# Performance work log

Hardware: AMD Instinct MI355X
Metric: run time of the kernel (lower is better)

The kernel has to match this reference:

```python
import jax, jax.numpy as jnp
import numpy as np
from jax.ops import segment_sum

N = 100000   # nodes
E = 6400000  # edges
D = 128      # input/output feature dim (d)
H = 15       # hidden width hard-coded in the module


def setup_inputs() -> dict:
    key = jax.random.key(0)
    ks = jax.random.split(key, 10)
    x = jax.random.normal(ks[0], (N, D), dtype=jnp.float32)
    edge_index = jax.random.randint(ks[1], (2, E), 0, N, dtype=jnp.int64)
    def glorot(k, shape):
        lim = np.sqrt(6.0 / (shape[0] + shape[1]))
        return jax.random.uniform(k, shape, jnp.float32, -lim, lim)
    W1 = glorot(ks[2], (D, H)); b1 = jnp.zeros((H,), jnp.float32)
    W2 = glorot(ks[3], (H, H)); b2 = jnp.zeros((H,), jnp.float32)
    W3 = glorot(ks[4], (H, H)); b3 = jnp.zeros((H,), jnp.float32)
    Wc = glorot(ks[5], (H, D)); bc = jnp.zeros((D,), jnp.float32)
    return {"x": x, "edge_index": edge_index,
            "W1": W1, "b1": b1, "W2": W2, "b2": b2,
            "W3": W3, "b3": b3, "Wc": Wc, "bc": bc}


def _gcn_norm(edge_index, n_nodes):
    # PyG GCNConv default: add self-loops, symmetric normalization.
    loops = jnp.arange(n_nodes, dtype=edge_index.dtype)
    row = jnp.concatenate([edge_index[0], loops])  # source
    col = jnp.concatenate([edge_index[1], loops])  # target (aggregation index)
    deg = segment_sum(jnp.ones_like(col, dtype=jnp.float32), col, num_segments=n_nodes)
    dinv = jnp.where(deg > 0, jax.lax.rsqrt(deg), 0.0)
    norm = dinv[row] * dinv[col]  # [E+N]
    return row, col, norm


def _gcn_conv(x, W, b, row, col, norm, n_nodes):
    h = x @ W                                   # [N, out]
    msg = h[row] * norm[:, None]                # gather + scale
    agg = segment_sum(msg, col, num_segments=n_nodes)
    return agg + b


def reference(x, edge_index, W1, b1, W2, b2, W3, b3, Wc, bc):
    row, col, norm = _gcn_norm(edge_index, N)
    h = jax.nn.relu(_gcn_conv(x, W1, b1, row, col, norm, N))
    h = jax.nn.relu(_gcn_conv(h, W2, b2, row, col, norm, N))
    h = jax.nn.relu(_gcn_conv(h, W3, b3, row, col, norm, N))
    return h @ Wc + bc
```

## Files before the change

kernel.cpp:

```cpp
#include <hip/hip_runtime.h>
#include <hip/hip_fp16.h>

#define DD 128
#define HH 15
#define BSHIFT 8
#define BUCK (1 << BSHIFT)
#define NBUCK 391
#define CAP 18432
#define CHUNK 4096
#define ABLK 512


__global__ __launch_bounds__(512) void init_gcur(int* __restrict__ gcur) {
    int i = threadIdx.x;
    if (i < NBUCK) gcur[i] = i * CAP;
}


__global__ __launch_bounds__(512) void partA(const int* __restrict__ row, const int* __restrict__ col,
                      int* __restrict__ gcur, unsigned* __restrict__ tmp, int E) {
    __shared__ int histo[NBUCK];
    __shared__ int hbase[NBUCK];
    __shared__ int hscan[NBUCK];
    __shared__ int wsum[8];
    __shared__ int s_total;
    __shared__ unsigned staged[CHUNK];
    __shared__ int saddr[CHUNK];
    int tid = threadIdx.x;
    int start = blockIdx.x * CHUNK;
    for (int i = tid; i < NBUCK; i += ABLK) histo[i] = 0;
    __syncthreads();
    unsigned pk[8]; unsigned short lp[8]; unsigned short bk[8];
    for (int k = 0; k < 8; ++k) {
        int e = start + k * ABLK + tid;
        bk[k] = 0xFFFF;
        if (e < E) {
            int cc = col[e];
            int b = cc >> BSHIFT;
            int rr = row[e];
            pk[k] = (unsigned)rr | ((unsigned)(cc & (BUCK - 1)) << 17);
            bk[k] = (unsigned short)b;
            lp[k] = (unsigned short)atomicAdd(&histo[b], 1);
        }
    }
    __syncthreads();
    int lane = tid & 63, wv = tid >> 6;
    int v = (tid < NBUCK) ? histo[tid] : 0;
    int s = v;
#pragma unroll
    for (int off = 1; off < 64; off <<= 1) {
        int u = __shfl_up(s, off, 64);
        if (lane >= off) s += u;
    }
    if (lane == 63) wsum[wv] = s;
    __syncthreads();
    if (tid == 0) {
        int r = 0;
        for (int i = 0; i < 8; ++i) { int u = wsum[i]; wsum[i] = r; r += u; }
        s_total = r;
    }
    __syncthreads();
    if (tid < NBUCK) {
        int excl = s + wsum[wv] - v;
        hscan[tid] = excl;
        if (v > 0) hbase[tid] = atomicAdd(&gcur[tid], v);
    }
    __syncthreads();
    for (int k = 0; k < 8; ++k) {
        if (bk[k] != 0xFFFF) {
            int b = bk[k];
            int slot = hscan[b] + lp[k];
            saddr[slot]  = min(hbase[b] + lp[k], NBUCK * CAP - 1);
            staged[slot] = pk[k];
        }
    }
    __syncthreads();
    int tot = s_total;
    for (int k = tid; k < tot; k += ABLK)
        tmp[saddr[k]] = staged[k];
}


__global__ __launch_bounds__(512) void scanC(const int* __restrict__ gcur,
                                             int* __restrict__ cbase,
                                             int* __restrict__ rowptr, int N) {
    __shared__ int wsum[8];
    int t = threadIdx.x, lane = t & 63, wv = t >> 6;
    int v = 0;
    if (t < NBUCK) v = min(gcur[t] - t * CAP, CAP);
    int s = v;
#pragma unroll
    for (int off = 1; off < 64; off <<= 1) {
        int u = __shfl_up(s, off, 64);
        if (lane >= off) s += u;
    }
    if (lane == 63) wsum[wv] = s;
    __syncthreads();
    int total = 0;
    if (t == 0) { int r = 0; for (int i = 0; i < 8; ++i) { int u = wsum[i]; wsum[i] = r; r += u; } total = r; }
    __syncthreads();
    if (t < NBUCK) cbase[t] = s + wsum[wv] - v;
    if (t == 0) { cbase[NBUCK] = total; rowptr[N] = total; }
}


__global__ __launch_bounds__(1024) void partB(const int* __restrict__ cbase, const unsigned* __restrict__ tmp,
                      int* __restrict__ rowptr, float* __restrict__ dinv,
                      int* __restrict__ csr_row, int N) {
    __shared__ int hist[BUCK];
    __shared__ int cur[BUCK];
    __shared__ int wsum[4];
    int b = blockIdx.x;
    int node0 = b << BSHIFT;
    int nn = min(BUCK, N - node0);
    int tid = threadIdx.x;
    if (tid < BUCK) hist[tid] = 0;
    __syncthreads();
    int base = cbase[b];
    int cnt  = cbase[b + 1] - base;
    const unsigned* te = tmp + (size_t)b * CAP;
    for (int e = tid; e < cnt; e += 1024)
        atomicAdd(&hist[te[e] >> 17], 1);
    __syncthreads();
    int lane = tid & 63, wv = tid >> 6;
    int d0 = (tid < BUCK) ? hist[tid] : 0;
    int s = d0;
#pragma unroll
    for (int off = 1; off < 64; off <<= 1) {
        int u = __shfl_up(s, off, 64);
        if (lane >= off) s += u;
    }
    if (tid < BUCK && lane == 63) wsum[wv] = s;
    __syncthreads();
    if (tid == 0) { int r = 0; for (int i = 0; i < 4; ++i) { int u = wsum[i]; wsum[i] = r; r += u; } }
    __syncthreads();
    if (tid < BUCK) {
        int excl = s + wsum[wv] - d0;
        cur[tid] = base + excl;
        if (tid < nn) {
            rowptr[node0 + tid] = base + excl;
            dinv[node0 + tid] = rsqrtf((float)(d0 + 1));
        }
    }
    __syncthreads();
    for (int e = tid; e < cnt; e += 1024) {
        unsigned v2 = te[e];
        int lc = (int)(v2 >> 17);
        int pos = atomicAdd(&cur[lc], 1);
        csr_row[pos] = (int)(v2 & 0x1FFFFu);
    }
}


__global__ void gemm1_kernel(const float* __restrict__ x, const float* __restrict__ W,
                             const float* __restrict__ dinv, __half* __restrict__ hs) {
    __shared__ float Wl[DD * HH];
    __shared__ float xs[16 * DD];
    int tid = threadIdx.x;
    for (int i = tid; i < DD * HH; i += 256) Wl[i] = W[i];
    size_t base = (size_t)blockIdx.x * 16 * DD;
    const float4* xv = (const float4*)(x + base);
    float4* xsv = (float4*)xs;
    xsv[tid]       = xv[tid];
    xsv[tid + 256] = xv[tid + 256];
    __syncthreads();
    int g = tid >> 4, f = tid & 15;
    int n = blockIdx.x * 16 + g;
    float val = 0.f;
    if (f < HH) {
        const float* xrow = xs + g * DD;
        float acc = 0.f;
#pragma unroll 8
        for (int k = 0; k < DD; ++k) acc += xrow[k] * Wl[k * HH + f];
        val = acc * dinv[n];
    }
    hs[(size_t)n * 16 + f] = __float2half(val);
}


__device__ inline void accU(float4& a0, float4& a1, const uint4& u) {
    float2 f0 = __half22float2(*(const __half2*)&u.x);
    float2 f1 = __half22float2(*(const __half2*)&u.y);
    float2 f2 = __half22float2(*(const __half2*)&u.z);
    float2 f3 = __half22float2(*(const __half2*)&u.w);
    a0.x += f0.x; a0.y += f0.y; a0.z += f1.x; a0.w += f1.y;
    a1.x += f2.x; a1.y += f2.y; a1.z += f3.x; a1.w += f3.y;
}

__device__ inline float4 shfl_down4(float4 v, int off) {
    v.x = __shfl_down(v.x, off, 64);
    v.y = __shfl_down(v.y, off, 64);
    v.z = __shfl_down(v.z, off, 64);
    v.w = __shfl_down(v.w, off, 64);
    return v;
}

template <int FUSE>
__global__ __launch_bounds__(256, 2)
void aggregate_kernel(const int* __restrict__ rowptr, const int* __restrict__ csr_row,
                      const float* __restrict__ dinv, const __half* __restrict__ hs,
                      float* __restrict__ aggout,
                      const float* __restrict__ bias, const float* __restrict__ W,
                      __half* __restrict__ hsout, int N) {
    __shared__ float Wl[16 * 16];
    __shared__ float bs[16];
    int tid = threadIdx.x;
    if (FUSE) {
        {
            int k = tid >> 4, f = tid & 15;
            Wl[tid] = (k < HH && f < HH) ? W[k * HH + f] : 0.f;
        }
        if (tid < 16) bs[tid] = (tid < HH) ? bias[tid] : 0.f;
        __syncthreads();
    }
    int wid = (blockIdx.x * 256 + tid) >> 6;
    int lane = tid & 63;
    int sub = lane & 15;
    int c = wid * 4 + (lane >> 4);
    int q = sub & 1, eg = sub >> 1;
    int s = 0, epe = 0;
    if (c < N) { s = rowptr[c]; epe = rowptr[c + 1]; }
    const uint4* h8 = (const uint4*)hs;
    float4 a0 = make_float4(0.f, 0.f, 0.f, 0.f), a1 = a0;
    int e = s + eg;
    for (; e + 56 < epe; e += 64) {
        int i0 = csr_row[e];      int i1 = csr_row[e + 8];
        int i2 = csr_row[e + 16]; int i3 = csr_row[e + 24];
        int i4 = csr_row[e + 32]; int i5 = csr_row[e + 40];
        int i6 = csr_row[e + 48]; int i7 = csr_row[e + 56];
        uint4 v0 = h8[((size_t)i0 << 1) + q];
        uint4 v1 = h8[((size_t)i1 << 1) + q];
        uint4 v2 = h8[((size_t)i2 << 1) + q];
        uint4 v3 = h8[((size_t)i3 << 1) + q];
        uint4 v4 = h8[((size_t)i4 << 1) + q];
        uint4 v5 = h8[((size_t)i5 << 1) + q];
        uint4 v6 = h8[((size_t)i6 << 1) + q];
        uint4 v7 = h8[((size_t)i7 << 1) + q];
        accU(a0, a1, v0); accU(a0, a1, v1); accU(a0, a1, v2); accU(a0, a1, v3);
        accU(a0, a1, v4); accU(a0, a1, v5); accU(a0, a1, v6); accU(a0, a1, v7);
    }
    for (; e + 8 < epe; e += 16) {
        int i0 = csr_row[e]; int i1 = csr_row[e + 8];
        uint4 v0 = h8[((size_t)i0 << 1) + q];
        uint4 v1 = h8[((size_t)i1 << 1) + q];
        accU(a0, a1, v0); accU(a0, a1, v1);
    }
    if (e < epe) {
        uint4 v0 = h8[((size_t)csr_row[e] << 1) + q];
        accU(a0, a1, v0);
    }
#define RED4(off) { float4 t0_ = shfl_down4(a0, off); float4 t1_ = shfl_down4(a1, off); \
                    a0.x += t0_.x; a0.y += t0_.y; a0.z += t0_.z; a0.w += t0_.w; \
                    a1.x += t1_.x; a1.y += t1_.y; a1.z += t1_.z; a1.w += t1_.w; }
    RED4(8) RED4(4) RED4(2)
#undef RED4
    float d = (c < N) ? dinv[c] : 0.f;
    float4 o0 = make_float4(0.f, 0.f, 0.f, 0.f), o1 = o0;
    if (sub < 2 && c < N) {
        uint4 su = h8[((size_t)c << 1) + q];
        float2 s0 = __half22float2(*(const __half2*)&su.x);
        float2 s1 = __half22float2(*(const __half2*)&su.y);
        float2 s2 = __half22float2(*(const __half2*)&su.z);
        float2 s3 = __half22float2(*(const __half2*)&su.w);
        o0.x = d * (a0.x + s0.x); o0.y = d * (a0.y + s0.y);
        o0.z = d * (a0.z + s1.x); o0.w = d * (a0.w + s1.y);
        o1.x = d * (a1.x + s2.x); o1.y = d * (a1.y + s2.y);
        o1.z = d * (a1.z + s3.x); o1.w = d * (a1.w + s3.y);
    }
    if (!FUSE) {
        if (sub < 2 && c < N) {
            ((float4*)aggout)[((size_t)c << 2) + q * 2]     = o0;
            ((float4*)aggout)[((size_t)c << 2) + q * 2 + 1] = o1;
        }
        return;
    }
    if (sub < 2) {
        int bb = q * 8;
        o0.x += bs[bb + 0]; o0.y += bs[bb + 1]; o0.z += bs[bb + 2]; o0.w += bs[bb + 3];
        o1.x += bs[bb + 4]; o1.y += bs[bb + 5]; o1.z += bs[bb + 6]; o1.w += bs[bb + 7];
        o0.x = fmaxf(o0.x, 0.f); o0.y = fmaxf(o0.y, 0.f);
        o0.z = fmaxf(o0.z, 0.f); o0.w = fmaxf(o0.w, 0.f);
        o1.x = fmaxf(o1.x, 0.f); o1.y = fmaxf(o1.y, 0.f);
        o1.z = fmaxf(o1.z, 0.f); o1.w = fmaxf(o1.w, 0.f);
    }
    int base = lane & ~15;
    float va[8], vb[8];
    va[0] = __shfl(o0.x, base, 64); va[1] = __shfl(o0.y, base, 64);
    va[2] = __shfl(o0.z, base, 64); va[3] = __shfl(o0.w, base, 64);
    va[4] = __shfl(o1.x, base, 64); va[5] = __shfl(o1.y, base, 64);
    va[6] = __shfl(o1.z, base, 64); va[7] = __shfl(o1.w, base, 64);
    vb[0] = __shfl(o0.x, base + 1, 64); vb[1] = __shfl(o0.y, base + 1, 64);
    vb[2] = __shfl(o0.z, base + 1, 64); vb[3] = __shfl(o0.w, base + 1, 64);
    vb[4] = __shfl(o1.x, base + 1, 64); vb[5] = __shfl(o1.y, base + 1, 64);
    vb[6] = __shfl(o1.z, base + 1, 64); vb[7] = __shfl(o1.w, base + 1, 64);
    float acc = 0.f;
#pragma unroll
    for (int k = 0; k < 8; ++k) acc += va[k] * Wl[k * 16 + sub];
#pragma unroll
    for (int k = 0; k < 8; ++k) acc += vb[k] * Wl[(8 + k) * 16 + sub];
    if (c < N) hsout[(size_t)c * 16 + sub] = __float2half(acc * d);
}


__global__ void gemm_out_kernel(const float* __restrict__ agg, const float* __restrict__ bias,
                                const float* __restrict__ Wc, const float* __restrict__ bc,
                                float* __restrict__ out, int N) {
    __shared__ float Wl[HH * DD];
    __shared__ float s_in[256];
    int tid = threadIdx.x;
    for (int i = tid; i < HH * DD; i += 256) Wl[i] = Wc[i];
    int n0 = blockIdx.x * 16;
    {
        int gg = tid >> 4, ff = tid & 15;
        int n = n0 + gg;
        float v = 0.f;
        if (ff < HH && n < N) v = agg[(size_t)n * 16 + ff] + bias[ff];
        s_in[tid] = v > 0.f ? v : 0.f;
    }
    __syncthreads();
    int g = tid >> 7, f = tid & 127;
    float bcf = bc[f];
#pragma unroll
    for (int it = 0; it < 8; ++it) {
        int nl = it * 2 + g;
        int n = n0 + nl;
        const float* in = s_in + nl * 16;
        float acc = bcf;
#pragma unroll
        for (int k = 0; k < HH; ++k) acc += in[k] * Wl[k * DD + f];
        if (n < N) out[(size_t)n * DD + f] = acc;
    }
}


extern "C" void kernel_launch(void* const* d_in, const int* in_sizes, int n_in,
                              void* d_out, int out_size, void* d_ws, size_t ws_size,
                              hipStream_t stream) {
    const float* x  = (const float*)d_in[0];
    const int*   ei = (const int*)d_in[1];
    const float* W1 = (const float*)d_in[2];
    const float* b1 = (const float*)d_in[3];
    const float* W2 = (const float*)d_in[4];
    const float* b2 = (const float*)d_in[5];
    const float* W3 = (const float*)d_in[6];
    const float* b3 = (const float*)d_in[7];
    const float* Wc = (const float*)d_in[8];
    const float* bc = (const float*)d_in[9];
    float* out = (float*)d_out;

    int N = in_sizes[0] / DD;
    int E = in_sizes[1] / 2;
    const int* row = ei;
    const int* col = ei + E;

    char* ws = (char*)d_ws;
    size_t off = 0;
    auto alloc = [&](size_t bytes) {
        void* p = ws + off;
        off += (bytes + 255) & ~(size_t)255;
        return p;
    };
    float*    dinv    = (float*)   alloc((size_t)N * 4);
    int*      rowptr  = (int*)     alloc((size_t)(N + 1) * 4);
    int*      gcur    = (int*)     alloc((size_t)NBUCK * 4);
    int*      cbase   = (int*)     alloc((size_t)(NBUCK + 1) * 4);
    int*      csr_row = (int*)     alloc((size_t)E * 4 + 256);
    unsigned* tmp     = (unsigned*)alloc((size_t)NBUCK * CAP * 4);
    (void)n_in; (void)out_size; (void)ws_size;

    __half* hsA = (__half*)tmp;
    __half* hsB = (__half*)((char*)tmp + (size_t)N * 32);
    float*  agg = (float*)((char*)tmp + (size_t)N * 64);

    int eblocks = (E + CHUNK - 1) / CHUNK;

    init_gcur<<<1, 512, 0, stream>>>(gcur);
    partA<<<eblocks, ABLK, 0, stream>>>(row, col, gcur, tmp, E);
    scanC<<<1, 512, 0, stream>>>(gcur, cbase, rowptr, N);
    partB<<<NBUCK, 1024, 0, stream>>>(cbase, tmp, rowptr, dinv, csr_row, N);

    int nb16 = (N + 15) / 16;
    int aggblocks = (N + 15) / 16;

    gemm1_kernel<<<nb16, 256, 0, stream>>>(x, W1, dinv, hsA);
    aggregate_kernel<1><<<aggblocks, 256, 0, stream>>>(rowptr, csr_row, dinv, hsA,
                                                       nullptr, b1, W2, hsB, N);
    aggregate_kernel<1><<<aggblocks, 256, 0, stream>>>(rowptr, csr_row, dinv, hsB,
                                                       nullptr, b2, W3, hsA, N);
    aggregate_kernel<0><<<aggblocks, 256, 0, stream>>>(rowptr, csr_row, dinv, hsA,
                                                       agg, nullptr, nullptr, nullptr, N);
    gemm_out_kernel<<<nb16, 256, 0, stream>>>(agg, b3, Wc, bc, out, N);
}
```

Measured before the change: 396.3 us.

## Fuse final aggregation with output GEMM and shrink partition chunks

```diff
diff --git a/kernel.cpp b/kernel.cpp
--- a/kernel.cpp
+++ b/kernel.cpp
@@ -7,8 +7,9 @@
 #define BUCK (1 << BSHIFT)
 #define NBUCK 391
 #define CAP 18432
-#define CHUNK 4096
-#define ABLK 512
+#define CHUNK 1042
+#define ABLK 256
+#define EPT 5
 
 
 __global__ __launch_bounds__(512) void init_gcur(int* __restrict__ gcur) {
@@ -17,12 +18,12 @@
 }
 
 
-__global__ __launch_bounds__(512) void partA(const int* __restrict__ row, const int* __restrict__ col,
+__global__ __launch_bounds__(256, 8) void partA(const int* __restrict__ row, const int* __restrict__ col,
                       int* __restrict__ gcur, unsigned* __restrict__ tmp, int E) {
     __shared__ int histo[NBUCK];
     __shared__ int hbase[NBUCK];
     __shared__ int hscan[NBUCK];
-    __shared__ int wsum[8];
+    __shared__ int wsum[4];
     __shared__ int s_total;
     __shared__ unsigned staged[CHUNK];
     __shared__ int saddr[CHUNK];
@@ -30,11 +31,12 @@
     int start = blockIdx.x * CHUNK;
     for (int i = tid; i < NBUCK; i += ABLK) histo[i] = 0;
     __syncthreads();
-    unsigned pk[8]; unsigned short lp[8]; unsigned short bk[8];
-    for (int k = 0; k < 8; ++k) {
-        int e = start + k * ABLK + tid;
+    unsigned pk[EPT]; unsigned short lp[EPT]; unsigned short bk[EPT];
+    for (int k = 0; k < EPT; ++k) {
+        int off = k * ABLK + tid;
+        int e = start + off;
         bk[k] = 0xFFFF;
-        if (e < E) {
+        if (off < CHUNK && e < E) {
             int cc = col[e];
             int b = cc >> BSHIFT;
             int rr = row[e];
@@ -45,7 +47,10 @@
     }
     __syncthreads();
     int lane = tid & 63, wv = tid >> 6;
-    int v = (tid < NBUCK) ? histo[tid] : 0;
+    int i0 = 2 * tid, i1 = 2 * tid + 1;
+    int h0 = (i0 < NBUCK) ? histo[i0] : 0;
+    int h1 = (i1 < NBUCK) ? histo[i1] : 0;
+    int v = h0 + h1;
     int s = v;
 #pragma unroll
     for (int off = 1; off < 64; off <<= 1) {
@@ -56,17 +61,21 @@
     __syncthreads();
     if (tid == 0) {
         int r = 0;
-        for (int i = 0; i < 8; ++i) { int u = wsum[i]; wsum[i] = r; r += u; }
+        for (int i = 0; i < 4; ++i) { int u = wsum[i]; wsum[i] = r; r += u; }
         s_total = r;
     }
     __syncthreads();
-    if (tid < NBUCK) {
-        int excl = s + wsum[wv] - v;
-        hscan[tid] = excl;
-        if (v > 0) hbase[tid] = atomicAdd(&gcur[tid], v);
-    }
-    __syncthreads();
-    for (int k = 0; k < 8; ++k) {
+    int excl = s + wsum[wv] - v;
+    if (i0 < NBUCK) {
+        hscan[i0] = excl;
+        if (h0 > 0) hbase[i0] = atomicAdd(&gcur[i0], h0);
+    }
+    if (i1 < NBUCK) {
+        hscan[i1] = excl + h0;
+        if (h1 > 0) hbase[i1] = atomicAdd(&gcur[i1], h1);
+    }
+    __syncthreads();
+    for (int k = 0; k < EPT; ++k) {
         if (bk[k] != 0xFFFF) {
             int b = bk[k];
             int slot = hscan[b] + lp[k];
@@ -196,21 +205,26 @@
 }
 
 template <int FUSE>
-__global__ __launch_bounds__(256, 2)
+__global__ __launch_bounds__(256, 5)
 void aggregate_kernel(const int* __restrict__ rowptr, const int* __restrict__ csr_row,
                       const float* __restrict__ dinv, const __half* __restrict__ hs,
-                      float* __restrict__ aggout,
                       const float* __restrict__ bias, const float* __restrict__ W,
-                      __half* __restrict__ hsout, int N) {
-    __shared__ float Wl[16 * 16];
+                      const float* __restrict__ bc,
+                      __half* __restrict__ hsout, float* __restrict__ outF, int N) {
+    __shared__ float Wl[FUSE == 2 ? HH * DD : 256];
     __shared__ float bs[16];
+    __shared__ float bcs[FUSE == 2 ? DD : 1];
+    __shared__ float sout[FUSE == 2 ? 16 * DD : 1];
     int tid = threadIdx.x;
-    if (FUSE) {
-        {
-            int k = tid >> 4, f = tid & 15;
-            Wl[tid] = (k < HH && f < HH) ? W[k * HH + f] : 0.f;
-        }
+    if (FUSE == 1) {
+        int k = tid >> 4, f = tid & 15;
+        Wl[tid] = (k < HH && f < HH) ? W[k * HH + f] : 0.f;
         if (tid < 16) bs[tid] = (tid < HH) ? bias[tid] : 0.f;
+        __syncthreads();
+    } else if (FUSE == 2) {
+        for (int i = tid; i < HH * DD; i += 256) Wl[i] = W[i];
+        if (tid < 16) bs[tid] = (tid < HH) ? bias[tid] : 0.f;
+        if (tid < DD) bcs[tid] = bc[tid];
         __syncthreads();
     }
     int wid = (blockIdx.x * 256 + tid) >> 6;
@@ -266,22 +280,11 @@
         o0.z = d * (a0.z + s1.x); o0.w = d * (a0.w + s1.y);
         o1.x = d * (a1.x + s2.x); o1.y = d * (a1.y + s2.y);
         o1.z = d * (a1.z + s3.x); o1.w = d * (a1.w + s3.y);
-    }
-    if (!FUSE) {
-        if (sub < 2 && c < N) {
-            ((float4*)aggout)[((size_t)c << 2) + q * 2]     = o0;
-            ((float4*)aggout)[((size_t)c << 2) + q * 2 + 1] = o1;
-        }
-        return;
-    }
-    if (sub < 2) {
         int bb = q * 8;
-        o0.x += bs[bb + 0]; o0.y += bs[bb + 1]; o0.z += bs[bb + 2]; o0.w += bs[bb + 3];
-        o1.x += bs[bb + 4]; o1.y += bs[bb + 5]; o1.z += bs[bb + 6]; o1.w += bs[bb + 7];
-        o0.x = fmaxf(o0.x, 0.f); o0.y = fmaxf(o0.y, 0.f);
-        o0.z = fmaxf(o0.z, 0.f); o0.w = fmaxf(o0.w, 0.f);
-        o1.x = fmaxf(o1.x, 0.f); o1.y = fmaxf(o1.y, 0.f);
-        o1.z = fmaxf(o1.z, 0.f); o1.w = fmaxf(o1.w, 0.f);
+        o0.x = fmaxf(o0.x + bs[bb + 0], 0.f); o0.y = fmaxf(o0.y + bs[bb + 1], 0.f);
+        o0.z = fmaxf(o0.z + bs[bb + 2], 0.f); o0.w = fmaxf(o0.w + bs[bb + 3], 0.f);
+        o1.x = fmaxf(o1.x + bs[bb + 4], 0.f); o1.y = fmaxf(o1.y + bs[bb + 5], 0.f);
+        o1.z = fmaxf(o1.z + bs[bb + 6], 0.f); o1.w = fmaxf(o1.w + bs[bb + 7], 0.f);
     }
     int base = lane & ~15;
     float va[8], vb[8];
@@ -293,42 +296,35 @@
     vb[2] = __shfl(o0.z, base + 1, 64); vb[3] = __shfl(o0.w, base + 1, 64);
     vb[4] = __shfl(o1.x, base + 1, 64); vb[5] = __shfl(o1.y, base + 1, 64);
     vb[6] = __shfl(o1.z, base + 1, 64); vb[7] = __shfl(o1.w, base + 1, 64);
-    float acc = 0.f;
-#pragma unroll
-    for (int k = 0; k < 8; ++k) acc += va[k] * Wl[k * 16 + sub];
-#pragma unroll
-    for (int k = 0; k < 8; ++k) acc += vb[k] * Wl[(8 + k) * 16 + sub];
-    if (c < N) hsout[(size_t)c * 16 + sub] = __float2half(acc * d);
-}
-
-
-__global__ void gemm_out_kernel(const float* __restrict__ agg, const float* __restrict__ bias,
-                                const float* __restrict__ Wc, const float* __restrict__ bc,
-                                float* __restrict__ out, int N) {
-    __shared__ float Wl[HH * DD];
-    __shared__ float s_in[256];
-    int tid = threadIdx.x;
-    for (int i = tid; i < HH * DD; i += 256) Wl[i] = Wc[i];
-    int n0 = blockIdx.x * 16;
-    {
-        int gg = tid >> 4, ff = tid & 15;
-        int n = n0 + gg;
-        float v = 0.f;
-        if (ff < HH && n < N) v = agg[(size_t)n * 16 + ff] + bias[ff];
-        s_in[tid] = v > 0.f ? v : 0.f;
-    }
-    __syncthreads();
-    int g = tid >> 7, f = tid & 127;
-    float bcf = bc[f];
-#pragma unroll
-    for (int it = 0; it < 8; ++it) {
-        int nl = it * 2 + g;
-        int n = n0 + nl;
-        const float* in = s_in + nl * 16;
-        float acc = bcf;
-#pragma unroll
-        for (int k = 0; k < HH; ++k) acc += in[k] * Wl[k * DD + f];
-        if (n < N) out[(size_t)n * DD + f] = acc;
+    if (FUSE == 1) {
+        float acc = 0.f;
+#pragma unroll
+        for (int k = 0; k < 8; ++k) acc += va[k] * Wl[k * 16 + sub];
+#pragma unroll
+        for (int k = 0; k < 8; ++k) acc += vb[k] * Wl[(8 + k) * 16 + sub];
+        if (c < N) hsout[(size_t)c * 16 + sub] = __float2half(acc * d);
+    } else if (FUSE == 2) {
+        int nl = (tid >> 4);
+#pragma unroll
+        for (int j = 0; j < 8; ++j) {
+            int f = sub + 16 * j;
+            float acc = bcs[f];
+#pragma unroll
+            for (int k = 0; k < 8; ++k)  acc += va[k] * Wl[k * DD + f];
+#pragma unroll
+            for (int k = 0; k < 7; ++k)  acc += vb[k] * Wl[(8 + k) * DD + f];
+            sout[nl * DD + f] = acc;
+        }
+        __syncthreads();
+        int n0 = blockIdx.x * 16;
+        const float4* sv = (const float4*)sout;
+#pragma unroll
+        for (int r = 0; r < 2; ++r) {
+            int idx = tid + 256 * r;
+            int node = idx >> 5, rem = idx & 31;
+            if (n0 + node < N)
+                ((float4*)outF)[((size_t)(n0 + node) * DD >> 2) + rem] = sv[idx];
+        }
     }
 }
 
@@ -370,7 +366,6 @@
 
     __half* hsA = (__half*)tmp;
     __half* hsB = (__half*)((char*)tmp + (size_t)N * 32);
-    float*  agg = (float*)((char*)tmp + (size_t)N * 64);
 
     int eblocks = (E + CHUNK - 1) / CHUNK;
 
@@ -384,10 +379,9 @@
 
     gemm1_kernel<<<nb16, 256, 0, stream>>>(x, W1, dinv, hsA);
     aggregate_kernel<1><<<aggblocks, 256, 0, stream>>>(rowptr, csr_row, dinv, hsA,
-                                                       nullptr, b1, W2, hsB, N);
+                                                       b1, W2, nullptr, hsB, nullptr, N);
     aggregate_kernel<1><<<aggblocks, 256, 0, stream>>>(rowptr, csr_row, dinv, hsB,
-                                                       nullptr, b2, W3, hsA, N);
-    aggregate_kernel<0><<<aggblocks, 256, 0, stream>>>(rowptr, csr_row, dinv, hsA,
-                                                       agg, nullptr, nullptr, nullptr, N);
-    gemm_out_kernel<<<nb16, 256, 0, stream>>>(agg, b3, Wc, bc, out, N);
-}
+                                                       b2, W3, nullptr, hsA, nullptr, N);
+    aggregate_kernel<2><<<aggblocks, 256, 0, stream>>>(rowptr, csr_row, dinv, hsA,
+                                                       b3, Wc, bc, nullptr, out, N);
+}
```

Result: slower. 587.0 us (+48.1%).
